# Optimization experiments

Measured on AMD Instinct MI355X. Metric: run time of the kernel, lower is better.

## Reference

```python
import jax, jax.numpy as jnp
import numpy as np

N_REL = 16   # n_relation
EMB = 512    # emb_size
N = 32768    # number of nodes/tokens


def setup_inputs() -> dict:
    key = jax.random.key(0)
    k1, k2, k3 = jax.random.split(key, 3)
    node_emb = jax.random.normal(k1, (N, EMB), dtype=jnp.float32)
    relation = jax.random.randint(k2, (N,), 0, N_REL)
    # nn.Linear default init: U(-1/sqrt(in_features), 1/sqrt(in_features))
    bound = 1.0 / np.sqrt(EMB)
    W = jax.random.uniform(k3, (N_REL, EMB, EMB), dtype=jnp.float32,
                           minval=-bound, maxval=bound)
    return {"node_emb": node_emb, "relation": relation, "W": W}


def reference(node_emb, relation, W):
    # out[i] = W[relation[i]] @ node_emb[i]  (F.linear(x, W_r) == x @ W_r.T)
    # Loop over the small fixed relation set via lax.scan; tokens stay vectorized.
    n_rel = W.shape[0]
    out0 = jnp.zeros((node_emb.shape[0], W.shape[1]), dtype=node_emb.dtype)

    def body(acc, wr):
        Wr, r = wr
        y = node_emb @ Wr.T                       # [N, EMB]
        acc = jnp.where((relation == r)[:, None], y, acc)
        return acc, None

    out, _ = jax.lax.scan(body, out0, (W, jnp.arange(n_rel)))
    return out
```

## Files before the change

kernel.cpp:

```cpp
#include <hip/hip_runtime.h>
#include <stdint.h>


#define EMB 512
#define N_RELC 16
#define BM 128
#define BN 128
#define BK 32
#define NKT (EMB / BK)

typedef __attribute__((ext_vector_type(4))) float f32x4;
typedef __attribute__((ext_vector_type(8))) short bf16x8;

__device__ __forceinline__ unsigned short f2bf(float f) {
  unsigned int u = __float_as_uint(f);
  u += 0x7FFFu + ((u >> 16) & 1u);
  return (unsigned short)(u >> 16);
}

__device__ __forceinline__ void gload_lds16(const void* g, void* l) {
  __builtin_amdgcn_global_load_lds(
      (const __attribute__((address_space(1))) unsigned int*)(uintptr_t)g,
      (__attribute__((address_space(3))) unsigned int*)(uintptr_t)l, 16, 0, 0);
}

__global__ void init_counts(int* cnt) {
  if (threadIdx.x < 32) cnt[threadIdx.x] = 0;
}

__global__ __launch_bounds__(256) void histo_rank_fill(
    const int* __restrict__ rel, int* cnt, int* pos, int* ptok,
    int n, int padn) {
  __shared__ int lcnt[N_RELC];
  __shared__ int lbase[N_RELC];
  const int tid = threadIdx.x;
  if (tid < N_RELC) lcnt[tid] = 0;
  __syncthreads();
  const int i = blockIdx.x * blockDim.x + tid;
  if (i < padn) ptok[i] = -1;
  int r = 0, myrank = 0;
  if (i < n) { r = rel[i]; myrank = atomicAdd(&lcnt[r], 1); }
  __syncthreads();
  if (tid < N_RELC) lbase[tid] = atomicAdd(&cnt[tid], lcnt[tid]);
  __syncthreads();
  if (i < n) pos[i] = lbase[r] + myrank;
}

__global__ void prefix_tiles64(const int* __restrict__ cnt, int* pbase,
                               int* tinfo, int maxt) {
  __shared__ int sb[N_RELC + 1];
  __shared__ int st[N_RELC + 1];
  if (threadIdx.x == 0) {
    int acc = 0, t = 0;
    for (int r = 0; r < N_RELC; ++r) {
      sb[r] = acc; st[r] = t;
      const int nt = (cnt[r] + BM - 1) / BM;
      acc += nt * BM;
      t += nt;
    }
    sb[N_RELC] = acc; st[N_RELC] = t;
  }
  __syncthreads();
  for (int i = threadIdx.x; i <= N_RELC; i += blockDim.x) pbase[i] = sb[i];
  for (int x = threadIdx.x; x < maxt; x += blockDim.x) {
    int v = -1;
    #pragma unroll
    for (int r = 0; r < N_RELC; ++r)
      if (x >= st[r] && x < st[r + 1]) v = (r << 16) | (x - st[r]);
    tinfo[x] = v;
  }
}

__global__ __launch_bounds__(256) void prep_all(
    const float* __restrict__ X, const float* __restrict__ W,
    const int* __restrict__ rel, const int* __restrict__ pos,
    const int* __restrict__ pbase, const int* __restrict__ cnt,
    unsigned short* __restrict__ Xs, unsigned short* __restrict__ Ws,
    int* __restrict__ ptok, int n, int welems, int gb)
{
  const int b = blockIdx.x;
  if (b < gb) {
    const int row = b * 4 + (threadIdx.x >> 6);
    const int lane = threadIdx.x & 63;
    if (row >= n) return;
    const int dst = pbase[rel[row]] + pos[row];
    if (lane == 0) ptok[dst] = row;
    const float* src = X + (size_t)row * EMB + lane * 8;
    f32x4 a = *reinterpret_cast<const f32x4*>(src);
    f32x4 c = *reinterpret_cast<const f32x4*>(src + 4);
    bf16x8 o;
    o[0] = f2bf(a[0]); o[1] = f2bf(a[1]); o[2] = f2bf(a[2]); o[3] = f2bf(a[3]);
    o[4] = f2bf(c[0]); o[5] = f2bf(c[1]); o[6] = f2bf(c[2]); o[7] = f2bf(c[3]);
    *reinterpret_cast<bf16x8*>(Xs + (size_t)dst * EMB + lane * 8) = o;
  } else if (b < gb + N_RELC) {
    const int r = b - gb;
    const int start = pbase[r] + cnt[r];
    const int end = pbase[r + 1];
    const int nvec = (end - start) * (EMB / 8);
    unsigned short* p = Xs + (size_t)start * EMB;
    const bf16x8 z = {0, 0, 0, 0, 0, 0, 0, 0};
    for (int v = threadIdx.x; v < nvec; v += blockDim.x)
      *reinterpret_cast<bf16x8*>(p + (size_t)v * 8) = z;
  } else {
    const size_t i = (((size_t)(b - gb - N_RELC)) * 256 + threadIdx.x) * 8;
    if (i >= (size_t)welems) return;
    f32x4 a = *reinterpret_cast<const f32x4*>(W + i);
    f32x4 c = *reinterpret_cast<const f32x4*>(W + i + 4);
    bf16x8 o;
    o[0] = f2bf(a[0]); o[1] = f2bf(a[1]); o[2] = f2bf(a[2]); o[3] = f2bf(a[3]);
    o[4] = f2bf(c[0]); o[5] = f2bf(c[1]); o[6] = f2bf(c[2]); o[7] = f2bf(c[3]);
    *reinterpret_cast<bf16x8*>(Ws + i) = o;
  }
}


#define STAGE(BUF, KT)                                                         \
  {                                                                            \
    const int kb_ = (KT) * BK;                                                 \
    gload_lds16(asrc0 + kb_, (char*)&As[BUF][0] + tid * 16);                   \
    gload_lds16(asrc1 + kb_, (char*)&As[BUF][0] + 4096 + tid * 16);            \
    gload_lds16(bsrc0 + kb_, (char*)&Bs[BUF][0] + tid * 16);                   \
    gload_lds16(bsrc1 + kb_, (char*)&Bs[BUF][0] + 4096 + tid * 16);            \
  }

#define COMPUTE(BUF)                                                           \
  {                                                                            \
    bf16x8 af[4], bfr[4];                                                      \
    _Pragma("unroll")                                                          \
    for (int m = 0; m < 4; ++m)                                                \
      af[m] = *reinterpret_cast<const bf16x8*>(                                \
          &As[BUF][(wr * 64 + m * 16 + lrow) * BK + gl * 8]);                  \
    _Pragma("unroll")                                                          \
    for (int nn = 0; nn < 4; ++nn)                                             \
      bfr[nn] = *reinterpret_cast<const bf16x8*>(                              \
          &Bs[BUF][(wc * 64 + nn * 16 + lrow) * BK + gl * 8]);                 \
    _Pragma("unroll")                                                          \
    for (int m = 0; m < 4; ++m)                                                \
      _Pragma("unroll")                                                        \
      for (int nn = 0; nn < 4; ++nn)                                           \
        acc[m][nn] = __builtin_amdgcn_mfma_f32_16x16x32_bf16(                  \
            af[m], bfr[nn], acc[m][nn], 0, 0, 0);                              \
  }

#define SYNC_STEP()                                                            \
  asm volatile("s_waitcnt vmcnt(0) lgkmcnt(0)" ::: "memory");                  \
  __builtin_amdgcn_s_barrier();                                                \
  __builtin_amdgcn_sched_barrier(0);

__global__ __launch_bounds__(256, 4) void gg6(
    const unsigned short* __restrict__ Xs, const unsigned short* __restrict__ Ws,
    const int* __restrict__ pbase, const int* __restrict__ tinfo,
    const int* __restrict__ ptok, float* __restrict__ out)
{
  __shared__ unsigned short As[2][BM * BK];
  __shared__ unsigned short Bs[2][BN * BK];

  const int info = tinfo[blockIdx.x];
  if (info < 0) return;
  const int r = info >> 16;
  const int mt = info & 0xFFFF;
  const int ct = blockIdx.y;
  const int prow0 = pbase[r] + mt * BM;

  const int tid = threadIdx.x;
  const int lane = tid & 63;
  const int wid = tid >> 6;
  const int wr = wid >> 1, wc = wid & 1;
  const int lrow = lane & 15;
  const int gl = lane >> 4;
  const int lrow4 = gl * 4;

  const unsigned short* asrc0 =
      Xs + (size_t)(prow0 + (tid >> 2)) * EMB + (tid & 3) * 8;
  const unsigned short* asrc1 = asrc0 + (size_t)64 * EMB;
  const unsigned short* bsrc0 =
      Ws + ((size_t)r * EMB + (size_t)(ct * BN + (tid >> 2))) * EMB + (tid & 3) * 8;
  const unsigned short* bsrc1 = bsrc0 + (size_t)64 * EMB;

  f32x4 acc[4][4];
  const f32x4 vzero = {0.f, 0.f, 0.f, 0.f};
  #pragma unroll
  for (int m = 0; m < 4; ++m)
    #pragma unroll
    for (int nn = 0; nn < 4; ++nn) acc[m][nn] = vzero;

  STAGE(0, 0);
  SYNC_STEP();

  #pragma unroll
  for (int kt2 = 0; kt2 < NKT / 2; ++kt2) {
    const int kte = kt2 * 2;
    if (kte + 1 < NKT) STAGE(1, kte + 1);
    COMPUTE(0);
    SYNC_STEP();
    if (kte + 2 < NKT) STAGE(0, kte + 2);
    COMPUTE(1);
    SYNC_STEP();
  }

  #pragma unroll
  for (int m = 0; m < 4; ++m) {
    const int base = prow0 + wr * 64 + m * 16 + lrow4;
    #pragma unroll
    for (int rg = 0; rg < 4; ++rg) {
      const int tok = ptok[base + rg];
      if (tok >= 0) {
        float* orow = out + (size_t)tok * EMB + ct * BN + wc * 64;
        #pragma unroll
        for (int nn = 0; nn < 4; ++nn)
          orow[nn * 16 + lrow] = acc[m][nn][rg];
      }
    }
  }
}

__global__ void naive_kernel(const float* __restrict__ X, const int* __restrict__ rel,
                             const float* __restrict__ W, float* __restrict__ out, int n) {
  int i = blockIdx.x;
  if (i >= n) return;
  int r = rel[i];
  const float* x = X + (size_t)i * EMB;
  const float* Wr = W + (size_t)r * EMB * EMB;
  for (int j = threadIdx.x; j < EMB; j += blockDim.x) {
    const float* w = Wr + (size_t)j * EMB;
    float s = 0.f;
    for (int k = 0; k < EMB; ++k) s += w[k] * x[k];
    out[(size_t)i * EMB + j] = s;
  }
}

extern "C" void kernel_launch(void* const* d_in, const int* in_sizes, int n_in,
                              void* d_out, int out_size, void* d_ws, size_t ws_size,
                              hipStream_t stream) {
  const float* X  = (const float*)d_in[0];
  const int* rel  = (const int*)d_in[1];
  const float* W  = (const float*)d_in[2];
  float* out      = (float*)d_out;
  const int n = in_sizes[1];
  const int welems = in_sizes[2];
  const int padn = n + N_RELC * BM;
  const int maxt = (n + BM - 1) / BM + N_RELC;
  const int maxtp = ((maxt + 7) / 8) * 8;

  const size_t ints = (size_t)64 + n + padn + maxtp;
  const size_t offW = ((ints * sizeof(int) + 255) / 256) * 256;
  const size_t offX = offW + (((size_t)welems * 2 + 255) / 256) * 256;
  const size_t need = offX + (size_t)padn * EMB * 2;

  if (ws_size < need) {
    naive_kernel<<<n, 256, 0, stream>>>(X, rel, W, out, n);
    return;
  }

  int* cnt   = (int*)d_ws;
  int* pbase = cnt + 16;
  int* pos   = cnt + 64;
  int* ptok  = pos + n;
  int* tinfo = ptok + padn;
  unsigned short* Ws = (unsigned short*)((char*)d_ws + offW);
  unsigned short* Xs = (unsigned short*)((char*)d_ws + offX);

  const int gb = (n + 3) / 4;
  const int wb = (welems / 8 + 255) / 256;

  init_counts<<<1, 32, 0, stream>>>(cnt);
  histo_rank_fill<<<(padn + 255) / 256, 256, 0, stream>>>(rel, cnt, pos, ptok, n, padn);
  prefix_tiles64<<<1, 64, 0, stream>>>(cnt, pbase, tinfo, maxtp);
  prep_all<<<gb + N_RELC + wb, 256, 0, stream>>>(X, W, rel, pos, pbase, cnt,
                                                 Xs, Ws, ptok, n, welems, gb);

  dim3 grid(maxtp, EMB / BN);
  gg6<<<grid, 256, 0, stream>>>(Xs, Ws, pbase, tinfo, ptok, out);
}
```

Measured before the change: 75.32 us.

## Triple-buffer GEMM LDS pipeline with partial vmcnt waits and swapped grid order

Replaces the double-buffered K loop with a three-stage LDS ring buffer. Loads are issued two tiles ahead, and the wait uses a partial vmcnt count instead of draining all memory operations every step. The grid is transposed so the four column tiles of one row tile launch consecutively, which should improve L2 reuse of the gathered X rows. The init_counts kernel is replaced with hipMemsetAsync. The cost is more LDS per block and an occupancy hint lowered from 4 to 3 blocks per CU.

```diff
diff --git a/kernel.cpp b/kernel.cpp
--- a/kernel.cpp
+++ b/kernel.cpp
@@ -7,7 +7,7 @@
 #define BM 128
 #define BN 128
 #define BK 32
-#define NKT (EMB / BK)
+#define NKT 16
 
 typedef __attribute__((ext_vector_type(4))) float f32x4;
 typedef __attribute__((ext_vector_type(8))) short bf16x8;
@@ -22,10 +22,6 @@
   __builtin_amdgcn_global_load_lds(
       (const __attribute__((address_space(1))) unsigned int*)(uintptr_t)g,
       (__attribute__((address_space(3))) unsigned int*)(uintptr_t)l, 16, 0, 0);
-}
-
-__global__ void init_counts(int* cnt) {
-  if (threadIdx.x < 32) cnt[threadIdx.x] = 0;
 }
 
 __global__ __launch_bounds__(256) void histo_rank_fill(
@@ -142,24 +138,31 @@
             af[m], bfr[nn], acc[m][nn], 0, 0, 0);                              \
   }
 
-#define SYNC_STEP()                                                            \
-  asm volatile("s_waitcnt vmcnt(0) lgkmcnt(0)" ::: "memory");                  \
-  __builtin_amdgcn_s_barrier();                                                \
-  __builtin_amdgcn_sched_barrier(0);
-
-__global__ __launch_bounds__(256, 4) void gg6(
+#define ITER(T, VM)                                                            \
+  {                                                                            \
+    if ((T) + 2 < NKT) STAGE(((T) + 2) % 3, (T) + 2);                          \
+    asm volatile("s_waitcnt vmcnt(" #VM ")" ::: "memory");                     \
+    __builtin_amdgcn_s_barrier();                                              \
+    __builtin_amdgcn_sched_barrier(0);                                         \
+    COMPUTE((T) % 3);                                                          \
+    asm volatile("s_waitcnt lgkmcnt(0)" ::: "memory");                         \
+    __builtin_amdgcn_s_barrier();                                              \
+    __builtin_amdgcn_sched_barrier(0);                                         \
+  }
+
+__global__ __launch_bounds__(256, 3) void gg8(
     const unsigned short* __restrict__ Xs, const unsigned short* __restrict__ Ws,
     const int* __restrict__ pbase, const int* __restrict__ tinfo,
     const int* __restrict__ ptok, float* __restrict__ out)
 {
-  __shared__ unsigned short As[2][BM * BK];
-  __shared__ unsigned short Bs[2][BN * BK];
-
-  const int info = tinfo[blockIdx.x];
+  __shared__ unsigned short As[3][BM * BK];
+  __shared__ unsigned short Bs[3][BN * BK];
+
+  const int info = tinfo[blockIdx.y];
   if (info < 0) return;
   const int r = info >> 16;
   const int mt = info & 0xFFFF;
-  const int ct = blockIdx.y;
+  const int ct = blockIdx.x;
   const int prow0 = pbase[r] + mt * BM;
 
   const int tid = threadIdx.x;
@@ -185,18 +188,12 @@
     for (int nn = 0; nn < 4; ++nn) acc[m][nn] = vzero;
 
   STAGE(0, 0);
-  SYNC_STEP();
-
-  #pragma unroll
-  for (int kt2 = 0; kt2 < NKT / 2; ++kt2) {
-    const int kte = kt2 * 2;
-    if (kte + 1 < NKT) STAGE(1, kte + 1);
-    COMPUTE(0);
-    SYNC_STEP();
-    if (kte + 2 < NKT) STAGE(0, kte + 2);
-    COMPUTE(1);
-    SYNC_STEP();
-  }
+  STAGE(1, 1);
+
+  ITER(0, 8)   ITER(1, 8)   ITER(2, 8)   ITER(3, 8)
+  ITER(4, 8)   ITER(5, 8)   ITER(6, 8)   ITER(7, 8)
+  ITER(8, 8)   ITER(9, 8)   ITER(10, 8)  ITER(11, 8)
+  ITER(12, 8)  ITER(13, 8)  ITER(14, 4)  ITER(15, 0)
 
   #pragma unroll
   for (int m = 0; m < 4; ++m) {
@@ -263,12 +260,12 @@
   const int gb = (n + 3) / 4;
   const int wb = (welems / 8 + 255) / 256;
 
-  init_counts<<<1, 32, 0, stream>>>(cnt);
+  hipMemsetAsync(cnt, 0, 64 * sizeof(int), stream);
   histo_rank_fill<<<(padn + 255) / 256, 256, 0, stream>>>(rel, cnt, pos, ptok, n, padn);
   prefix_tiles64<<<1, 64, 0, stream>>>(cnt, pbase, tinfo, maxtp);
   prep_all<<<gb + N_RELC + wb, 256, 0, stream>>>(X, W, rel, pos, pbase, cnt,
                                                  Xs, Ws, ptok, n, welems, gb);
 
-  dim3 grid(maxtp, EMB / BN);
-  gg6<<<grid, 256, 0, stream>>>(Xs, Ws, pbase, tinfo, ptok, out);
-}
+  dim3 grid(EMB / BN, maxtp);
+  gg8<<<grid, 256, 0, stream>>>(Xs, Ws, pbase, tinfo, ptok, out);
+}
```

New measurement: 76.31 us. No clear change (+1.3%).
